# Kernel tuning notes

Measured on AMD Instinct MI355X. Metric: run time of the kernel, lower is better.

The kernel has to match this reference:

```python
import jax, jax.numpy as jnp
import numpy as np
from jax import lax

T, B, D, H, L, NDIR = 512, 64, 512, 512, 3, 2

def _lengths():
    return 512 - 4 * np.arange(64)  # per-sequence lengths, non-increasing

def _qdq(w):
    # simulate dynamic int8 symmetric per-tensor weight quantization
    s = jnp.max(jnp.abs(w)) / 127.0
    return jnp.clip(jnp.round(w / s), -127, 127) * s

def setup_inputs() -> dict:
    key = jax.random.key(0)
    ks = jax.random.split(key, 9)
    lengths = _lengths()
    bs = np.array([(lengths > t).sum() for t in range(T)], dtype=np.int64)  # [T]
    pack_idx = np.concatenate([t * B + np.arange(bs[t]) for t in range(T)]).astype(np.int32)
    sc = 0.05
    data = jax.random.normal(ks[0], (int(bs.sum()), D), jnp.float32)
    h0 = jax.random.normal(ks[1], (L * NDIR, B, H), jnp.float32)
    c0 = jax.random.normal(ks[2], (L * NDIR, B, H), jnp.float32)
    w_ih0 = _qdq(jax.random.normal(ks[3], (NDIR, 4 * H, D)) * sc)
    w_hh0 = _qdq(jax.random.normal(ks[4], (NDIR, 4 * H, H)) * sc)
    b0 = jax.random.normal(ks[5], (NDIR, 4 * H)) * sc  # b_ih + b_hh combined
    w_ih_r = _qdq(jax.random.normal(ks[6], (L - 1, NDIR, 4 * H, NDIR * H)) * sc)
    w_hh_r = _qdq(jax.random.normal(ks[7], (L - 1, NDIR, 4 * H, H)) * sc)
    b_r = jax.random.normal(ks[8], (L - 1, NDIR, 4 * H)) * sc
    return {"data": data, "h0": h0, "c0": c0, "w_ih0": w_ih0, "w_hh0": w_hh0, "b0": b0,
            "w_ih_r": w_ih_r, "w_hh_r": w_hh_r, "b_r": b_r,
            "batch_sizes": jnp.asarray(bs), "pack_idx": jnp.asarray(pack_idx)}

def _run_dir(x, mask, h0, c0, w_ih, w_hh, b):
    # x: [T,B,in], mask: [T,B]; batch the input GEMM over all timesteps
    gx = jnp.einsum('tbd,gd->tbg', x, w_ih) + b  # [T,B,4H]
    def step(carry, inp):
        h, c = carry
        gx_t, m = inp
        gates = gx_t + h @ w_hh.T
        i, f, g, o = jnp.split(gates, 4, axis=-1)  # PyTorch gate order i,f,g,o
        c_new = jax.nn.sigmoid(f) * c + jax.nn.sigmoid(i) * jnp.tanh(g)
        h_new = jax.nn.sigmoid(o) * jnp.tanh(c_new)
        m = m[:, None]
        return (jnp.where(m, h_new, h), jnp.where(m, c_new, c)), jnp.where(m, h_new, h)
    (hT, cT), ys = lax.scan(step, (h0, c0), (gx, mask))
    return ys * mask[:, :, None], hT, cT

def _lstm(data, h0, c0, w_ih0, w_hh0, b0, w_ih_r, w_hh_r, b_r, batch_sizes, pack_idx):
    mask = jnp.arange(B)[None, :] < batch_sizes[:, None]          # [T,B] valid slots
    lengths = jnp.sum(mask, axis=0)                                # [B]
    rev_idx = jnp.clip(lengths[None, :] - 1 - jnp.arange(T)[:, None], 0, T - 1)  # [T,B]
    barange = jnp.arange(B)[None, :]
    x = jnp.zeros((T * B, D), data.dtype).at[pack_idx].set(data).reshape(T, B, D)
    h_ns, c_ns = [], []
    for l in range(L):
        outs = []
        for d in range(NDIR):
            if l == 0:
                w_ih, w_hh, b = w_ih0[d], w_hh0[d], b0[d]
            else:
                w_ih, w_hh, b = w_ih_r[l - 1, d], w_hh_r[l - 1, d], b_r[l - 1, d]
            hi, ci = h0[NDIR * l + d], c0[NDIR * l + d]
            if d == 0:
                ys, hT, cT = _run_dir(x, mask, hi, ci, w_ih, w_hh, b)
            else:
                x_rev = x[rev_idx, barange]               # per-sequence reversal
                ys_r, hT, cT = _run_dir(x_rev, mask, hi, ci, w_ih, w_hh, b)
                ys = ys_r[rev_idx, barange] * mask[:, :, None]
            outs.append(ys); h_ns.append(hT); c_ns.append(cT)
        x = jnp.concatenate(outs, axis=-1)  # [T,B,2H] feeds next layer
    out = x.reshape(T * B, NDIR * H)[pack_idx]  # repack to [total_tokens, 2H]
    return out, jnp.stack(h_ns), jnp.stack(c_ns)

def reference(data, h0, c0, w_ih0, w_hh0, b0, w_ih_r, w_hh_r, b_r, batch_sizes, pack_idx):
    return _lstm(data, h0, c0, w_ih0, w_hh0, b0, w_ih_r, w_hh_r, b_r, batch_sizes, pack_idx)
```

## Files before the change

kernel.cpp:

```cpp
#include <hip/hip_runtime.h>
#include <cmath>

typedef _Float16 f16;
typedef _Float16 half8 __attribute__((ext_vector_type(8)));
typedef float floatx4 __attribute__((ext_vector_type(4)));
typedef unsigned u32x4 __attribute__((ext_vector_type(4)));

#define NT 512
#define NB 64
#define NH 512
#define NG 2048
#define CHUNK 128

__device__ inline float sigf(float x) { return 1.0f / (1.0f + __expf(-x)); }
__device__ inline float tanhfast(float x) { return 2.0f / (1.0f + __expf(-2.0f * x)) - 1.0f; }

__device__ inline void load_lds16(const f16* g, f16* l) {
  __builtin_amdgcn_global_load_lds(
      (__attribute__((address_space(1))) void*)g,
      (__attribute__((address_space(3))) void*)l, 16, 0, 0);
}

__global__ void prep_meta(const int* __restrict__ bs_raw, int* __restrict__ lens,
                          int* __restrict__ cum) {
  __shared__ int sbs[NT];
  int stride = (bs_raw[1] == 0) ? 2 : 1;
  for (int i = threadIdx.x; i < NT; i += 256) sbs[i] = bs_raw[i * stride];
  __syncthreads();
  for (int b = threadIdx.x; b < NB; b += 256) {
    int n = 0;
    for (int t = 0; t < NT; ++t) n += (sbs[t] > b);
    lens[b] = n;
  }
  if (threadIdx.x == 0) {
    int run = 0;
    for (int t = 0; t < NT; ++t) { cum[t] = run; run += sbs[t]; }
  }
}

__global__ void scatter_rows(const float* __restrict__ data, const int* __restrict__ pidx,
                             f16* __restrict__ X0) {
  int r = blockIdx.x;
  int row = pidx[r];
  const float* src = data + (size_t)r * 512;
  f16* dst = X0 + (size_t)row * 512;
  for (int k = threadIdx.x; k < 512; k += 256) dst[k] = (f16)src[k];
}

__global__ void f32_to_f16(const float* __restrict__ in, f16* __restrict__ out, size_t n) {
  size_t i = (size_t)blockIdx.x * 256 + threadIdx.x;
  size_t stride = (size_t)gridDim.x * 256;
  for (; i < n; i += stride) out[i] = (f16)in[i];
}

__global__ void init_h(const float* __restrict__ h0, const float* __restrict__ c0,
                       float* __restrict__ hsave, float* __restrict__ csave,
                       unsigned* __restrict__ ht, int layer) {
  int idx = blockIdx.x * 256 + threadIdx.x;
  int d = idx >> 15, rem = idx & 32767;
  float hv = h0[(size_t)(2 * layer + d) * NB * NH + rem];
  float cv = c0[(size_t)(2 * layer + d) * NB * NH + rem];
  hsave[idx] = hv;
  csave[idx] = cv;
  union { f16 f; unsigned short s; } hc; hc.f = (f16)hv;
  unsigned word = ((unsigned)(layer * NT) << 16) | hc.s;
  __hip_atomic_store(ht + (size_t)d * NB * NH + rem, word,
                     __ATOMIC_RELAXED, __HIP_MEMORY_SCOPE_AGENT);
}

__global__ __launch_bounds__(256) void gemm_gx(const f16* __restrict__ A,
                                               const f16* __restrict__ W,
                                               const float* __restrict__ bias,
                                               const int* __restrict__ lens,
                                               f16* __restrict__ gxc, int K, int c0) {
  const int d = blockIdx.z;
  const int m0 = blockIdx.y * 128;
  const int n0 = blockIdx.x * 128;
  const f16* Wd = W + (size_t)d * NG * K;

  __shared__ __align__(16) f16 As[128 * 32];
  __shared__ __align__(16) f16 Bs[128 * 32];

  const int tid = threadIdx.x, lane = tid & 63, wv = tid >> 6;
  const int wm = wv >> 1, wn = wv & 1;
  const int lrow = lane >> 2, lcol = (lane & 3) * 8;
  const int q = lane >> 4, nn = lane & 15;

  const f16* aptr[2];
  const f16* bptr[2];
#pragma unroll
  for (int i = 0; i < 2; ++i) {
    int ch = wv * 2 + i;
    int m = m0 + ch * 16 + lrow;
    int t = c0 + (m >> 6), b = m & 63;
    int tt = t;
    if (d) { tt = lens[b] - 1 - t; tt = tt < 0 ? 0 : (tt > NT - 1 ? NT - 1 : tt); }
    aptr[i] = A + (size_t)(tt * NB + b) * K + lcol;
    bptr[i] = Wd + (size_t)(n0 + ch * 16 + lrow) * K + lcol;
  }

  floatx4 acc[4][4] = {};
  for (int k0 = 0; k0 < K; k0 += 32) {
    __syncthreads();
#pragma unroll
    for (int i = 0; i < 2; ++i) {
      int ch = wv * 2 + i;
      load_lds16(aptr[i] + k0, As + ch * 512);
      load_lds16(bptr[i] + k0, Bs + ch * 512);
    }
    __syncthreads();
    half8 a[4], b[4];
#pragma unroll
    for (int f = 0; f < 4; ++f) {
      a[f] = *(const half8*)(As + (wm * 64 + f * 16 + nn) * 32 + q * 8);
      b[f] = *(const half8*)(Bs + (wn * 64 + f * 16 + nn) * 32 + q * 8);
    }
#pragma unroll
    for (int fm = 0; fm < 4; ++fm)
#pragma unroll
      for (int fn = 0; fn < 4; ++fn)
        acc[fm][fn] = __builtin_amdgcn_mfma_f32_16x16x32_f16(a[fm], b[fn], acc[fm][fn], 0, 0, 0);
  }

  f16* gxd = gxc + (size_t)d * CHUNK * NB * NG;
#pragma unroll
  for (int fn = 0; fn < 4; ++fn) {
    int col = n0 + wn * 64 + fn * 16 + nn;
    float bv = bias[d * NG + col];
#pragma unroll
    for (int fm = 0; fm < 4; ++fm) {
      int mb = m0 + wm * 64 + fm * 16 + q * 4;
#pragma unroll
      for (int r = 0; r < 4; ++r)
        gxd[(size_t)(mb + r) * NG + col] = (f16)(acc[fm][fn][r] + bv);
    }
  }
}

__global__ __launch_bounds__(256, 1) void lstm_rec(
    const f16* __restrict__ gxc, const f16* __restrict__ whh,
    const int* __restrict__ lens, const int* __restrict__ cum,
    float* __restrict__ hsave, float* __restrict__ csave,
    unsigned* __restrict__ ht, f16* __restrict__ Y, float* __restrict__ outp,
    float* __restrict__ hT, float* __restrict__ cT,
    int c0, int mode, int layer) {
  const int tid = threadIdx.x, lane = tid & 63, wv = tid >> 6;
  const int g = blockIdx.x & 7, w = blockIdx.x >> 3;
  const int dir = g & 1, bsl = g >> 1;
  const int q = lane >> 4, nn = lane & 15;

  const int maxlen = lens[bsl * 16];
  int nst = maxlen - c0;
  if (nst <= 0) return;
  if (nst > CHUNK) nst = CHUNK;

  __shared__ __align__(16) unsigned As[2][16][260];
  __shared__ float s_g[4][16][17];

  const int jbase = w * 16 + wv * 4;
  const int coln = (nn >> 2) * NH + jbase + (nn & 3);
  const f16* whd = whh + (size_t)dir * NG * NH;
  half8 bf[16];
#pragma unroll
  for (int s = 0; s < 16; ++s)
    bf[s] = *(const half8*)(whd + (size_t)coln * NH + s * 32 + q * 8);

  const int b_e = bsl * 16 + nn;
  const int jglob = jbase + q;
  const int lene = lens[b_e];
  const int brow = bsl * 16 + q * 4;
  const int lidx = (dir * NB + b_e) * NH + jglob;
  float h = hsave[lidx], c = csave[lidx];

  const f16* gxd = gxc + (size_t)dir * CHUNK * NB * NG;
  const int ebase = layer * NT;

  for (int ct = 0; ct < nst; ++ct) {
    const int t = c0 + ct;
    const int e = ebase + t;
    const int par = t & 1;

    float gxv[4];
#pragma unroll
    for (int r = 0; r < 4; ++r)
      gxv[r] = (float)gxd[(size_t)(ct * NB + brow + r) * NG + coln];

    const unsigned long long* p64 =
        (const unsigned long long*)(ht + ((size_t)(par * 2 + dir) * NB + bsl * 16 + nn) * NH +
                                    wv * 128 + q * 8);
    unsigned long long wb[4][4];
    bool done[4] = {false, false, false, false};
    int it = 0;
    for (;;) {
#pragma unroll
      for (int s = 0; s < 4; ++s)
        if (!done[s]) {
#pragma unroll
          for (int i = 0; i < 4; ++i)
            wb[s][i] = __hip_atomic_load(p64 + s * 16 + i, __ATOMIC_RELAXED,
                                         __HIP_MEMORY_SCOPE_AGENT);
          unsigned tg = 0xffffu;
#pragma unroll
          for (int i = 0; i < 4; ++i) {
            tg &= (unsigned)(wb[s][i] >> 16) & 0xffffu;
            tg &= (unsigned)(wb[s][i] >> 48);
          }
          done[s] = (tg >= (unsigned)e);
        }
      bool ok = done[0] & done[1] & done[2] & done[3];
      if (__ballot(ok) == ~0ull) break;
      if (++it > 100000) break;
    }

#pragma unroll
    for (int s = 0; s < 4; ++s) {
      unsigned d0 = (unsigned)(wb[s][0] & 0xffffu) | ((unsigned)(wb[s][0] >> 32) << 16);
      unsigned d1 = (unsigned)(wb[s][1] & 0xffffu) | ((unsigned)(wb[s][1] >> 32) << 16);
      unsigned d2 = (unsigned)(wb[s][2] & 0xffffu) | ((unsigned)(wb[s][2] >> 32) << 16);
      unsigned d3 = (unsigned)(wb[s][3] & 0xffffu) | ((unsigned)(wb[s][3] >> 32) << 16);
      *(u32x4*)&As[par][nn][wv * 64 + s * 16 + q * 4] = (u32x4){d0, d1, d2, d3};
    }
    __syncthreads();

    floatx4 acc0 = {0.f, 0.f, 0.f, 0.f}, acc1 = {0.f, 0.f, 0.f, 0.f};
#pragma unroll
    for (int s = 0; s < 8; ++s) {
      half8 a0 = *(const half8*)&As[par][nn][(2 * s) * 16 + q * 4];
      half8 a1 = *(const half8*)&As[par][nn][(2 * s + 1) * 16 + q * 4];
      acc0 = __builtin_amdgcn_mfma_f32_16x16x32_f16(a0, bf[2 * s], acc0, 0, 0, 0);
      acc1 = __builtin_amdgcn_mfma_f32_16x16x32_f16(a1, bf[2 * s + 1], acc1, 0, 0, 0);
    }
#pragma unroll
    for (int r = 0; r < 4; ++r) s_g[wv][q * 4 + r][nn] = acc0[r] + acc1[r] + gxv[r];

    const bool act = (t < lene);
    if (act) {
      float gi = s_g[wv][nn][q];
      float gf = s_g[wv][nn][4 + q];
      float gg = s_g[wv][nn][8 + q];
      float go = s_g[wv][nn][12 + q];
      c = sigf(gf) * c + sigf(gi) * tanhfast(gg);
      h = sigf(go) * tanhfast(c);
    }
    union { f16 f; unsigned short s; } hc; hc.f = (f16)h;
    unsigned word = ((unsigned)(e + 1) << 16) | hc.s;
    __hip_atomic_store(ht + ((size_t)(((t + 1) & 1) * 2 + dir) * NB + b_e) * NH + jglob,
                       word, __ATOMIC_RELAXED, __HIP_MEMORY_SCOPE_AGENT);
    if (mode == 0) {
      int tp = act ? (dir ? (lene - 1 - t) : t) : t;
      Y[(size_t)(tp * NB + b_e) * (2 * NH) + dir * NH + jglob] = act ? (f16)h : (f16)0.f;
    } else if (act) {
      int tp = dir ? (lene - 1 - t) : t;
      outp[(size_t)(cum[tp] + b_e) * (2 * NH) + dir * NH + jglob] = h;
    }
  }

  hsave[lidx] = h;
  csave[lidx] = c;
  const int sidx = ((2 * layer + dir) * NB + b_e) * NH + jglob;
  hT[sidx] = h;
  cT[sidx] = c;
}

extern "C" void kernel_launch(void* const* d_in, const int* in_sizes, int n_in,
                              void* d_out, int out_size, void* d_ws, size_t ws_size,
                              hipStream_t stream) {
  const float* data  = (const float*)d_in[0];
  const float* h0    = (const float*)d_in[1];
  const float* c0    = (const float*)d_in[2];
  const float* w_ih0 = (const float*)d_in[3];
  const float* w_hh0 = (const float*)d_in[4];
  const float* b0    = (const float*)d_in[5];
  const float* w_ihr = (const float*)d_in[6];
  const float* w_hhr = (const float*)d_in[7];
  const float* b_r   = (const float*)d_in[8];
  const int* bs_raw  = (const int*)d_in[9];
  const int* pidx    = (const int*)d_in[10];
  const int nrows = in_sizes[0] / 512;
  float* out = (float*)d_out;

  f16* Y0 = (f16*)d_out;
  float* hT = out + (size_t)nrows * 1024;
  float* cT = hT + (size_t)6 * NB * NH;

  char* p = (char*)d_ws;
  auto take = [&](size_t bytes) {
    char* r = p;
    p += (bytes + 255) & ~(size_t)255;
    return (void*)r;
  };
  f16* gxc   = (f16*)take((size_t)2 * CHUNK * NB * NG * 2);
  f16* Y1    = (f16*)take((size_t)NT * NB * 1024 * 2);
  f16* X0    = Y1;
  f16* wih16 = (f16*)take((size_t)2 * NG * 1024 * 2);
  f16* whh16 = (f16*)take((size_t)2 * NG * NH * 2);
  unsigned* ht = (unsigned*)take((size_t)2 * 2 * NB * NH * 4);
  float* hsave = (float*)take((size_t)2 * NB * NH * 4);
  float* csave = (float*)take((size_t)2 * NB * NH * 4);
  int* lens = (int*)take(256);
  int* cum  = (int*)take(NT * 4);

  prep_meta<<<1, 256, 0, stream>>>(bs_raw, lens, cum);
  (void)hipMemsetAsync(X0, 0, (size_t)NT * NB * 512 * 2, stream);
  (void)hipMemsetAsync(ht, 0, (size_t)2 * 2 * NB * NH * 4, stream);
  scatter_rows<<<nrows, 256, 0, stream>>>(data, pidx, X0);

  for (int l = 0; l < 3; ++l) {
    const float* wih_f = (l == 0) ? w_ih0 : w_ihr + (size_t)(l - 1) * 2 * NG * 1024;
    const float* whh_f = (l == 0) ? w_hh0 : w_hhr + (size_t)(l - 1) * 2 * NG * NH;
    const float* bias  = (l == 0) ? b0 : b_r + (size_t)(l - 1) * 2 * NG;
    const int K = (l == 0) ? 512 : 1024;
    const f16* Xl = (l == 0) ? X0 : ((l == 1) ? Y0 : Y1);
    f16* Yl = (l == 0) ? Y0 : Y1;
    f32_to_f16<<<256, 256, 0, stream>>>(wih_f, wih16, (size_t)2 * NG * K);
    f32_to_f16<<<256, 256, 0, stream>>>(whh_f, whh16, (size_t)2 * NG * NH);
    init_h<<<256, 256, 0, stream>>>(h0, c0, hsave, csave, ht, l);
    for (int c = 0; c < 4; ++c) {
      gemm_gx<<<dim3(16, 64, 2), 256, 0, stream>>>(Xl, wih16, bias, lens, gxc, K, c * CHUNK);
      lstm_rec<<<256, 256, 0, stream>>>(gxc, whh16, lens, cum, hsave, csave, ht, Yl,
                                        out, hT, cT, c * CHUNK, (l == 2) ? 1 : 0, l);
    }
  }
}
```

Before: 8.295 ms.

## Poll compact per-block step counters before reading tagged hidden-state words

New measurement: 7.122 ms. 14.1% less time.

```diff
diff --git a/kernel.cpp b/kernel.cpp
--- a/kernel.cpp
+++ b/kernel.cpp
@@ -55,7 +55,7 @@
 
 __global__ void init_h(const float* __restrict__ h0, const float* __restrict__ c0,
                        float* __restrict__ hsave, float* __restrict__ csave,
-                       unsigned* __restrict__ ht, int layer) {
+                       unsigned* __restrict__ ht, unsigned* __restrict__ ctr, int layer) {
   int idx = blockIdx.x * 256 + threadIdx.x;
   int d = idx >> 15, rem = idx & 32767;
   float hv = h0[(size_t)(2 * layer + d) * NB * NH + rem];
@@ -66,6 +66,10 @@
   unsigned word = ((unsigned)(layer * NT) << 16) | hc.s;
   __hip_atomic_store(ht + (size_t)d * NB * NH + rem, word,
                      __ATOMIC_RELAXED, __HIP_MEMORY_SCOPE_AGENT);
+  if (blockIdx.x == 0) {
+    __hip_atomic_store(ctr + threadIdx.x, (unsigned)(layer * NT),
+                       __ATOMIC_RELAXED, __HIP_MEMORY_SCOPE_AGENT);
+  }
 }
 
 __global__ __launch_bounds__(256) void gemm_gx(const f16* __restrict__ A,
@@ -141,7 +145,8 @@
     const f16* __restrict__ gxc, const f16* __restrict__ whh,
     const int* __restrict__ lens, const int* __restrict__ cum,
     float* __restrict__ hsave, float* __restrict__ csave,
-    unsigned* __restrict__ ht, f16* __restrict__ Y, float* __restrict__ outp,
+    unsigned* __restrict__ ht, unsigned* __restrict__ ctr,
+    f16* __restrict__ Y, float* __restrict__ outp,
     float* __restrict__ hT, float* __restrict__ cT,
     int c0, int mode, int layer) {
   const int tid = threadIdx.x, lane = tid & 63, wv = tid >> 6;
@@ -175,6 +180,8 @@
   const f16* gxd = gxc + (size_t)dir * CHUNK * NB * NG;
   const int ebase = layer * NT;
 
+  const unsigned* cslot = ctr + (size_t)g * 32 + (lane & 31);
+
   for (int ct = 0; ct < nst; ++ct) {
     const int t = c0 + ct;
     const int e = ebase + t;
@@ -185,39 +192,44 @@
     for (int r = 0; r < 4; ++r)
       gxv[r] = (float)gxd[(size_t)(ct * NB + brow + r) * NG + coln];
 
+    {
+      const unsigned* cp = cslot + par * 256;
+      int it = 0;
+      for (;;) {
+        unsigned cv = __hip_atomic_load(cp, __ATOMIC_RELAXED, __HIP_MEMORY_SCOPE_AGENT);
+        if (__ballot((int)cv >= e) == ~0ull) break;
+        if (++it > 500000) break;
+      }
+    }
+
     const unsigned long long* p64 =
         (const unsigned long long*)(ht + ((size_t)(par * 2 + dir) * NB + bsl * 16 + nn) * NH +
                                     wv * 128 + q * 8);
-    unsigned long long wb[4][4];
-    bool done[4] = {false, false, false, false};
-    int it = 0;
-    for (;;) {
-#pragma unroll
-      for (int s = 0; s < 4; ++s)
-        if (!done[s]) {
-#pragma unroll
-          for (int i = 0; i < 4; ++i)
-            wb[s][i] = __hip_atomic_load(p64 + s * 16 + i, __ATOMIC_RELAXED,
-                                         __HIP_MEMORY_SCOPE_AGENT);
-          unsigned tg = 0xffffu;
-#pragma unroll
-          for (int i = 0; i < 4; ++i) {
-            tg &= (unsigned)(wb[s][i] >> 16) & 0xffffu;
-            tg &= (unsigned)(wb[s][i] >> 48);
-          }
-          done[s] = (tg >= (unsigned)e);
+    unsigned long long wb[16];
+    {
+      int it = 0;
+      for (;;) {
+#pragma unroll
+        for (int i = 0; i < 16; ++i)
+          wb[i] = __hip_atomic_load(p64 + (i >> 2) * 16 + (i & 3), __ATOMIC_RELAXED,
+                                    __HIP_MEMORY_SCOPE_AGENT);
+        unsigned tg = 0xffffu;
+#pragma unroll
+        for (int i = 0; i < 16; ++i) {
+          tg &= (unsigned)(wb[i] >> 16) & 0xffffu;
+          tg &= (unsigned)(wb[i] >> 48);
         }
-      bool ok = done[0] & done[1] & done[2] & done[3];
-      if (__ballot(ok) == ~0ull) break;
-      if (++it > 100000) break;
+        if (__ballot(tg >= (unsigned)e) == ~0ull) break;
+        if (++it > 100000) break;
+      }
     }
 
 #pragma unroll
     for (int s = 0; s < 4; ++s) {
-      unsigned d0 = (unsigned)(wb[s][0] & 0xffffu) | ((unsigned)(wb[s][0] >> 32) << 16);
-      unsigned d1 = (unsigned)(wb[s][1] & 0xffffu) | ((unsigned)(wb[s][1] >> 32) << 16);
-      unsigned d2 = (unsigned)(wb[s][2] & 0xffffu) | ((unsigned)(wb[s][2] >> 32) << 16);
-      unsigned d3 = (unsigned)(wb[s][3] & 0xffffu) | ((unsigned)(wb[s][3] >> 32) << 16);
+      unsigned d0 = (unsigned)(wb[4 * s + 0] & 0xffffu) | ((unsigned)(wb[4 * s + 0] >> 32) << 16);
+      unsigned d1 = (unsigned)(wb[4 * s + 1] & 0xffffu) | ((unsigned)(wb[4 * s + 1] >> 32) << 16);
+      unsigned d2 = (unsigned)(wb[4 * s + 2] & 0xffffu) | ((unsigned)(wb[4 * s + 2] >> 32) << 16);
+      unsigned d3 = (unsigned)(wb[4 * s + 3] & 0xffffu) | ((unsigned)(wb[4 * s + 3] >> 32) << 16);
       *(u32x4*)&As[par][nn][wv * 64 + s * 16 + q * 4] = (u32x4){d0, d1, d2, d3};
     }
     __syncthreads();
@@ -246,6 +258,9 @@
     unsigned word = ((unsigned)(e + 1) << 16) | hc.s;
     __hip_atomic_store(ht + ((size_t)(((t + 1) & 1) * 2 + dir) * NB + b_e) * NH + jglob,
                        word, __ATOMIC_RELAXED, __HIP_MEMORY_SCOPE_AGENT);
+    if (tid == 0)
+      __hip_atomic_store(ctr + (size_t)(((t + 1) & 1) * 256 + g * 32 + w), (unsigned)(e + 1),
+                         __ATOMIC_RELAXED, __HIP_MEMORY_SCOPE_AGENT);
     if (mode == 0) {
       int tp = act ? (dir ? (lene - 1 - t) : t) : t;
       Y[(size_t)(tp * NB + b_e) * (2 * NH) + dir * NH + jglob] = act ? (f16)h : (f16)0.f;
@@ -295,6 +310,7 @@
   f16* wih16 = (f16*)take((size_t)2 * NG * 1024 * 2);
   f16* whh16 = (f16*)take((size_t)2 * NG * NH * 2);
   unsigned* ht = (unsigned*)take((size_t)2 * 2 * NB * NH * 4);
+  unsigned* ctr = (unsigned*)take((size_t)2 * 8 * 32 * 4);
   float* hsave = (float*)take((size_t)2 * NB * NH * 4);
   float* csave = (float*)take((size_t)2 * NB * NH * 4);
   int* lens = (int*)take(256);
@@ -303,6 +319,7 @@
   prep_meta<<<1, 256, 0, stream>>>(bs_raw, lens, cum);
   (void)hipMemsetAsync(X0, 0, (size_t)NT * NB * 512 * 2, stream);
   (void)hipMemsetAsync(ht, 0, (size_t)2 * 2 * NB * NH * 4, stream);
+  (void)hipMemsetAsync(ctr, 0, (size_t)2 * 8 * 32 * 4, stream);
   scatter_rows<<<nrows, 256, 0, stream>>>(data, pidx, X0);
 
   for (int l = 0; l < 3; ++l) {
@@ -314,10 +331,10 @@
     f16* Yl = (l == 0) ? Y0 : Y1;
     f32_to_f16<<<256, 256, 0, stream>>>(wih_f, wih16, (size_t)2 * NG * K);
     f32_to_f16<<<256, 256, 0, stream>>>(whh_f, whh16, (size_t)2 * NG * NH);
-    init_h<<<256, 256, 0, stream>>>(h0, c0, hsave, csave, ht, l);
+    init_h<<<256, 256, 0, stream>>>(h0, c0, hsave, csave, ht, ctr, l);
     for (int c = 0; c < 4; ++c) {
       gemm_gx<<<dim3(16, 64, 2), 256, 0, stream>>>(Xl, wih16, bias, lens, gxc, K, c * CHUNK);
-      lstm_rec<<<256, 256, 0, stream>>>(gxc, whh16, lens, cum, hsave, csave, ht, Yl,
+      lstm_rec<<<256, 256, 0, stream>>>(gxc, whh16, lens, cum, hsave, csave, ht, ctr, Yl,
                                         out, hT, cT, c * CHUNK, (l == 2) ? 1 : 0, l);
     }
   }
```
